# Kernel optimization log

Hardware: AMD Instinct MI355X
Metric: run time of the kernel (lower is better)

Reference implementation:

```python
import jax, jax.numpy as jnp
import numpy as np

B, M, D = 8, 1024, 1024
H = 16
HD = D // H  # 64
F = 4096

def layer_norm(x, gamma, beta, eps=1e-5):
    mu = jnp.mean(x, axis=-1, keepdims=True)
    var = jnp.var(x, axis=-1, keepdims=True)
    return (x - mu) * jax.lax.rsqrt(var + eps) * gamma + beta

def setup_inputs() -> dict:
    key = jax.random.key(0)
    ks = jax.random.split(key, 16)
    s = 0.02
    return {
        "h": jax.random.normal(ks[0], (B, M, D), jnp.float32),
        "h_all": jax.random.normal(ks[1], (B, M, D), jnp.float32),
        "Wq": jax.random.normal(ks[2], (D, D), jnp.float32) * s,
        "Wk": jax.random.normal(ks[3], (D, D), jnp.float32) * s,
        "Wv": jax.random.normal(ks[4], (D, D), jnp.float32) * s,
        "Wo": jax.random.normal(ks[5], (D, D), jnp.float32) * s,
        "W1": jax.random.normal(ks[6], (D, F), jnp.float32) * s,
        "b1": jnp.zeros((F,), jnp.float32),
        "W2": jax.random.normal(ks[7], (F, D), jnp.float32) * s,
        "b2": jnp.zeros((D,), jnp.float32),
        "g1": jnp.ones((D,), jnp.float32),
        "be1": jnp.zeros((D,), jnp.float32),
        "g2": jnp.ones((D,), jnp.float32),
        "be2": jnp.zeros((D,), jnp.float32),
    }

def reference(h, h_all, Wq, Wk, Wv, Wo, W1, b1, W2, b2, g1, be1, g2, be2):
    Bx, Mx, Dx = h.shape
    # projections (no bias, per nn.Linear(bias=False))
    q = (h @ Wq).reshape(Bx, Mx, H, HD)        # [B,M,H,hd]
    k = (h_all @ Wk).reshape(Bx, -1, H, HD)    # [B,N,H,hd]
    v = (h_all @ Wv).reshape(Bx, -1, H, HD)
    # attention: scale by sqrt(head_dim) as in SeqAttention(hidden_size=head_dim)
    scores = jnp.einsum('bqhd,bkhd->bhqk', q, k) / jnp.sqrt(jnp.float32(HD))
    attn = jax.nn.softmax(scores, axis=-1)
    ctx = jnp.einsum('bhqk,bkhd->bqhd', attn, v).reshape(Bx, Mx, Dx)
    attn_out = ctx @ Wo
    # post-norm residual 1
    h1 = layer_norm(h + attn_out, g1, be1)
    # FFN
    ff = jax.nn.relu(h1 @ W1 + b1) @ W2 + b2
    # post-norm residual 2
    out = layer_norm(h1 + ff, g2, be2)
    return out
```

## Files before the change

### kernel.cpp

```cpp
#include <hip/hip_runtime.h>
#include <hip/hip_bf16.h>

#define ROWS 8192
#define DD   1024
#define HH   16
#define HD   64
#define FF   4096

typedef __attribute__((ext_vector_type(4))) float f32x4;
typedef __attribute__((ext_vector_type(8))) __bf16 bf16x8;

static __device__ __forceinline__ unsigned short f2bf(float f) {
  unsigned u = __float_as_uint(f);
  u += 0x7fffu + ((u >> 16) & 1u);
  return (unsigned short)(u >> 16);
}

static __device__ __forceinline__ float bf2f(unsigned short u) {
  return __uint_as_float(((unsigned)u) << 16);
}

static __device__ __forceinline__ unsigned cvtpk_bf16(float lo, float hi) {
  unsigned r;
  asm("v_cvt_pk_bf16_f32 %0, %1, %2" : "=v"(r) : "v"(lo), "v"(hi));
  return r;
}

static __device__ __forceinline__ f32x4 mfma16(bf16x8 a, bf16x8 b, f32x4 c) {
  return __builtin_amdgcn_mfma_f32_16x16x32_bf16(a, b, c, 0, 0, 0);
}

#define GLOAD16(gp, lp) __builtin_amdgcn_global_load_lds( \
    (__attribute__((address_space(1))) void*)(gp), \
    (__attribute__((address_space(3))) void*)(lp), 16, 0, 0)

__global__ __launch_bounds__(256) void prep_k(
    const float* __restrict__ h, const float* __restrict__ hall,
    const float* __restrict__ Wq, const float* __restrict__ Wk,
    const float* __restrict__ Wv, const float* __restrict__ Wo,
    const float* __restrict__ W1, const float* __restrict__ W2,
    unsigned short* __restrict__ hb, unsigned short* __restrict__ hab,
    unsigned short* __restrict__ wqt, unsigned short* __restrict__ wkvt,
    unsigned short* __restrict__ wot, unsigned short* __restrict__ w1t,
    unsigned short* __restrict__ w2t) {
  __shared__ float tile[32][33];
  const int bid = blockIdx.x;
  const int tid = threadIdx.x;

  if (bid < 16384) {
    const float* src = (bid < 8192) ? h : hall;
    unsigned short* dst = (bid < 8192) ? hb : hab;
    int i = (bid & 8191) * 256 + tid;
    float4 v = ((const float4*)src)[i];
    ushort4 o;
    o.x = f2bf(v.x); o.y = f2bf(v.y); o.z = f2bf(v.z); o.w = f2bf(v.w);
    ((ushort4*)dst)[i] = o;
    return;
  }

  int r = bid - 16384;
  const float* src; unsigned short* dst; int R, C, bx, by;
  if (r < 4096) {
    int which = r >> 10, idx = r & 1023;
    R = C = 1024; bx = idx & 31; by = idx >> 5;
    if (which == 0) { src = Wq; dst = wqt; }
    else if (which == 1) { src = Wk; dst = wkvt; }
    else if (which == 2) { src = Wv; dst = wkvt + (size_t)DD * DD; }
    else { src = Wo; dst = wot; }
  } else if (r < 8192) {
    int idx = r - 4096;
    R = 1024; C = 4096; bx = idx & 127; by = idx >> 7;
    src = W1; dst = w1t;
  } else {
    int idx = r - 8192;
    R = 4096; C = 1024; bx = idx & 31; by = idx >> 5;
    src = W2; dst = w2t;
  }
  const int tx = tid & 31, ty = tid >> 5;
  #pragma unroll
  for (int i = 0; i < 32; i += 8)
    tile[ty + i][tx] = src[(size_t)(by * 32 + ty + i) * C + bx * 32 + tx];
  __syncthreads();
  #pragma unroll
  for (int i = 0; i < 32; i += 8)
    dst[(size_t)(bx * 32 + ty + i) * R + by * 32 + tx] = f2bf(tile[tx][ty + i]);
}

template <int BM, int MODE, int KS = 1>
__global__ __launch_bounds__(512, 2) void gemm256(
    const unsigned short* __restrict__ A, const unsigned short* __restrict__ BT,
    const float* __restrict__ bias, void* __restrict__ Cout, void* __restrict__ Cout2,
    int Ni, int Ki, int nbx) {
  constexpr int MR = BM / 32;

  const int tid  = threadIdx.x;
  const int lane = tid & 63;
  const int wid  = tid >> 6;
  const int wm   = wid >> 2;
  const int wn   = wid & 3;
  const int lr   = lane & 15;
  const int kq   = lane >> 4;

  const int nwg = gridDim.x;
  const int cpx = nwg >> 3;
  const int wg  = (int)blockIdx.x;
  const int swz = (wg & 7) * cpx + (wg >> 3);
  const int perk = nwg / KS;
  const int kh   = swz / perk;
  const int swzr = swz % perk;
  const int bx = swzr % nbx, by = swzr / nbx;
  const int brow = by * BM, bcol = bx * 256;
  const int Kc   = Ki / KS;
  const int kbase = kh * Kc;

  f32x4 acc[MR][4] = {};
  const int NT = Kc >> 6;

  if constexpr (BM == 256) {
    __shared__ unsigned short As[2 * 2 * 256 * 32];
    __shared__ unsigned short Bs[2 * 2 * 256 * 32];

    const int srow0 = tid >> 2;
    const int csw   = ((tid & 3) ^ ((tid >> 3) & 3)) * 8;
    const size_t sA0 = (size_t)(brow + srow0) * Ki + kbase + csw;
    const size_t sB0 = (size_t)(bcol + srow0) * Ki + kbase + csw;
    const int coff = ((kq ^ ((lr >> 1) & 3)) << 4);

    auto stageu = [&](int srcT, int db, int ks) {
      const size_t so = (size_t)srcT * 64 + ks * 32;
      char* la = (char*)As + (db * 2 + ks) * 16384 + wid * 1024;
      char* lb = (char*)Bs + (db * 2 + ks) * 16384 + wid * 1024;
      GLOAD16(A + sA0 + so, la);
      GLOAD16(A + sA0 + so + (size_t)128 * Ki, la + 8192);
      GLOAD16(BT + sB0 + so, lb);
      GLOAD16(BT + sB0 + so + (size_t)128 * Ki, lb + 8192);
    };

    stageu(0, 0, 0);
    stageu(0, 0, 1);
    stageu(1, 1, 0);

    #pragma unroll 1
    for (int t = 0; t < NT; ++t) {
      const int d = t & 1;
      #pragma unroll
      for (int p = 0; p < 2; ++p) {
        asm volatile("s_waitcnt vmcnt(8)" ::: "memory");
        __builtin_amdgcn_s_barrier();
        __builtin_amdgcn_sched_barrier(0);
        const char* ab = (const char*)As + (d * 2 + p) * 16384;
        const char* bb = (const char*)Bs + (d * 2 + p) * 16384;
        bf16x8 af[8], bfv[4];
        #pragma unroll
        for (int m = 0; m < 8; ++m)
          af[m] = *(const bf16x8*)(ab + (wm * 128 + m * 16 + lr) * 64 + coff);
        #pragma unroll
        for (int n = 0; n < 4; ++n)
          bfv[n] = *(const bf16x8*)(bb + (wn * 64 + n * 16 + lr) * 64 + coff);
        if (p == 0) {
          const int ts = (t + 1 < NT) ? t + 1 : NT - 1;
          stageu(ts, (t + 1) & 1, 1);
        } else {
          const int ts = (t + 2 < NT) ? t + 2 : NT - 1;
          stageu(ts, d, 0);
        }
        __builtin_amdgcn_s_setprio(1);
        #pragma unroll
        for (int m = 0; m < 8; ++m)
          #pragma unroll
          for (int n = 0; n < 4; ++n)
            acc[m][n] = mfma16(af[m], bfv[n], acc[m][n]);
        __builtin_amdgcn_s_setprio(0);
      }
    }
    asm volatile("s_waitcnt vmcnt(0)" ::: "memory");
  } else {
    __shared__ unsigned short As[2][BM * 64];
    __shared__ unsigned short Bs[2][256 * 64];
    const int axor = (lr & 7) << 4;
    const int srow = wid * 8 + (lane >> 3);
    const int scol = ((lane & 7) * 8) ^ ((srow & 7) << 3);
    size_t offA[BM / 64], offB[4];
    #pragma unroll
    for (int L = 0; L < BM / 64; ++L)
      offA[L] = (size_t)(brow + L * 64 + srow) * Ki + kbase + scol;
    #pragma unroll
    for (int L = 0; L < 4; ++L)
      offB[L] = (size_t)(bcol + L * 64 + srow) * Ki + kbase + scol;

    auto stage = [&](int t, int d) {
      #pragma unroll
      for (int L = 0; L < BM / 64; ++L)
        GLOAD16(A + offA[L] + t * 64, (char*)As[d] + L * 8192 + wid * 1024);
      #pragma unroll
      for (int L = 0; L < 4; ++L)
        GLOAD16(BT + offB[L] + t * 64, (char*)Bs[d] + L * 8192 + wid * 1024);
    };

    stage(0, 0);
    stage(1, 1);

    #pragma unroll 1
    for (int t = 0; t < NT; ++t) {
      const int d = t & 1;
      asm volatile("s_waitcnt vmcnt(6)" ::: "memory");
      __builtin_amdgcn_s_barrier();
      __builtin_amdgcn_sched_barrier(0);

      const unsigned short* as = As[d];
      const unsigned short* bs = Bs[d];
      #pragma unroll
      for (int kk = 0; kk < 2; ++kk) {
        bf16x8 af[MR], bfv[4];
        #pragma unroll
        for (int m = 0; m < MR; ++m)
          af[m] = *(const bf16x8*)((const char*)as +
              (wm * (BM / 2) + m * 16 + lr) * 128 + ((kk * 64 + kq * 16) ^ axor));
        #pragma unroll
        for (int n = 0; n < 4; ++n)
          bfv[n] = *(const bf16x8*)((const char*)bs +
              (wn * 64 + n * 16 + lr) * 128 + ((kk * 64 + kq * 16) ^ axor));
        #pragma unroll
        for (int m = 0; m < MR; ++m)
          #pragma unroll
          for (int n = 0; n < 4; ++n)
            acc[m][n] = mfma16(af[m], bfv[n], acc[m][n]);
      }

      asm volatile("s_waitcnt lgkmcnt(0)" ::: "memory");
      __builtin_amdgcn_s_barrier();
      __builtin_amdgcn_sched_barrier(0);
      const int ts = (t + 2 < NT) ? t + 2 : NT - 1;
      stage(ts, d);
    }
  }

  #pragma unroll
  for (int m = 0; m < MR; ++m) {
    #pragma unroll
    for (int n = 0; n < 4; ++n) {
      const int r0 = brow + wm * (BM / 2) + m * 16 + kq * 4;
      const int c  = bcol + wn * 64 + n * 16 + lr;
      if constexpr (MODE == 4) {
        if (c < 1024) {
          #pragma unroll
          for (int e = 0; e < 4; ++e)
            ((unsigned short*)Cout)[(size_t)(r0 + e) * 1024 + c] = f2bf(acc[m][n][e]);
        } else {
          const int cc = c - 1024;
          const int bq = r0 >> 10;
          const int tok = r0 & 1023;
          ushort4 pk;
          pk.x = f2bf(acc[m][n][0]); pk.y = f2bf(acc[m][n][1]);
          pk.z = f2bf(acc[m][n][2]); pk.w = f2bf(acc[m][n][3]);
          *(ushort4*)((unsigned short*)Cout2 + ((size_t)bq * 1024 + cc) * 1024 + tok) = pk;
        }
      } else if constexpr (MODE == 5) {
        if (kh == 0) {
          const float bv = bias[c];
          #pragma unroll
          for (int e = 0; e < 4; ++e)
            ((float*)Cout)[(size_t)(r0 + e) * Ni + c] = acc[m][n][e] + bv;
        } else {
          #pragma unroll
          for (int e = 0; e < 4; ++e)
            ((unsigned short*)Cout2)[(size_t)(r0 + e) * Ni + c] = f2bf(acc[m][n][e]);
        }
      } else {
        const float bv = (MODE == 2 || MODE == 3) ? bias[c] : 0.0f;
        #pragma unroll
        for (int e = 0; e < 4; ++e) {
          float v = acc[m][n][e] + bv;
          if (MODE == 2) v = fmaxf(v, 0.0f);
          if (MODE == 0 || MODE == 2)
            ((unsigned short*)Cout)[(size_t)(r0 + e) * Ni + c] = f2bf(v);
          else
            ((float*)Cout)[(size_t)(r0 + e) * Ni + c] = v;
        }
      }
    }
  }
}

__global__ __launch_bounds__(512, 6) void attn_k(
    const unsigned short* __restrict__ q, const unsigned short* __restrict__ k,
    const unsigned short* __restrict__ vT, unsigned short* __restrict__ ctx) {
  __shared__ unsigned short Ks[2][64 * 64];
  __shared__ unsigned short Vt[2][64 * 64];
  __shared__ unsigned short Ps[8][16 * 64];
  const int tid = threadIdx.x;
  const int lane = tid & 63;
  const int wid = tid >> 6;
  const int bh = blockIdx.x;
  const int b = bh >> 4, h = bh & 15;
  const int qrow0 = blockIdx.y * 128 + wid * 16;
  const size_t tokbase = (size_t)b * 1024;
  const int lr = lane & 15, kq = lane >> 4;

  const int srow = tid >> 3;
  const int scol = ((tid & 7) * 8) ^ ((srow & 7) << 3);
  const unsigned short* kg = k + (tokbase + srow) * 1024 + h * 64 + scol;
  const unsigned short* vg = vT + ((size_t)(b * 16 + h) * 64 + srow) * 1024 + scol;
  const int ldst = tid * 16;

  auto stage = [&](int kt, int d) {
    GLOAD16(kg + (size_t)kt * 64 * 1024, (char*)Ks[d] + ldst);
    GLOAD16(vg + kt * 64, (char*)Vt[d] + ldst);
  };

  bf16x8 aq[2];
  {
    const unsigned short* qp = q + (tokbase + qrow0 + lr) * DD + h * 64 + kq * 8;
    aq[0] = *(const bf16x8*)qp;
    aq[1] = *(const bf16x8*)(qp + 32);
  }

  float l_acc = 0.f;
  f32x4 acc[4] = {};
  const float C = 0.125f * 1.4426950408889634f;
  const unsigned swp = (unsigned)((lr & 7) << 4);
  const unsigned pbase = (unsigned)(lr * 128);

  stage(0, 0);
  stage(1, 1);

  #pragma unroll 2
  for (int kt = 0; kt < 16; ++kt) {
    const int d = kt & 1;
    asm volatile("s_waitcnt vmcnt(2)" ::: "memory");
    __builtin_amdgcn_s_barrier();
    __builtin_amdgcn_sched_barrier(0);

    f32x4 sv[4] = {};
    #pragma unroll
    for (int jb = 0; jb < 4; ++jb)
      #pragma unroll
      for (int ks = 0; ks < 2; ++ks) {
        int row = jb * 16 + lr;
        bf16x8 ak = *(const bf16x8*)((const char*)Ks[d] +
            row * 128 + ((ks * 64 + kq * 16) ^ ((row & 7) << 4)));
        sv[jb] = mfma16(ak, aq[ks], sv[jb]);
      }

    #pragma unroll
    for (int jb = 0; jb < 4; ++jb) {
      float p0 = exp2f(sv[jb][0] * C);
      float p1 = exp2f(sv[jb][1] * C);
      float p2 = exp2f(sv[jb][2] * C);
      float p3 = exp2f(sv[jb][3] * C);
      l_acc += (p0 + p1) + (p2 + p3);
      uint2 w;
      w.x = cvtpk_bf16(p0, p1);
      w.y = cvtpk_bf16(p2, p3);
      unsigned off = pbase + (((unsigned)(jb * 32 + kq * 8)) ^ swp);
      *(uint2*)((char*)Ps[wid] + off) = w;
    }

    #pragma unroll
    for (int ks = 0; ks < 2; ++ks) {
      bf16x8 ap = *(const bf16x8*)((const char*)Ps[wid] +
          lr * 128 + ((ks * 64 + kq * 16) ^ ((lr & 7) << 4)));
      #pragma unroll
      for (int db = 0; db < 4; ++db) {
        int dd = db * 16 + lr;
        bf16x8 bv = *(const bf16x8*)((const char*)Vt[d] +
            dd * 128 + ((ks * 64 + kq * 16) ^ ((dd & 7) << 4)));
        acc[db] = mfma16(bv, ap, acc[db]);
      }
    }

    asm volatile("s_waitcnt lgkmcnt(0)" ::: "memory");
    __builtin_amdgcn_s_barrier();
    __builtin_amdgcn_sched_barrier(0);
    const int ts = (kt + 2 < 16) ? kt + 2 : 15;
    stage(ts, d);
  }

  float l = l_acc + __shfl_xor(l_acc, 16);
  l += __shfl_xor(l, 32);
  const float inv = 1.0f / l;
  unsigned short* cp = ctx + (tokbase + qrow0 + lr) * DD + h * 64 + kq * 4;
  #pragma unroll
  for (int db = 0; db < 4; ++db) {
    ushort4 o;
    o.x = f2bf(acc[db][0] * inv);
    o.y = f2bf(acc[db][1] * inv);
    o.z = f2bf(acc[db][2] * inv);
    o.w = f2bf(acc[db][3] * inv);
    *(ushort4*)(cp + db * 16) = o;
  }
}

__global__ __launch_bounds__(256) void ln_add_bb_k(
    const unsigned short* __restrict__ a, const unsigned short* __restrict__ b,
    const float* __restrict__ gamma, const float* __restrict__ beta,
    unsigned short* __restrict__ outb) {
  int row = blockIdx.x;
  int tid = threadIdx.x;
  size_t base = (size_t)row * 1024 + tid * 4;
  ushort4 va = *(const ushort4*)(a + base);
  ushort4 vb = *(const ushort4*)(b + base);
  float x[4] = {bf2f(va.x) + bf2f(vb.x), bf2f(va.y) + bf2f(vb.y),
                bf2f(va.z) + bf2f(vb.z), bf2f(va.w) + bf2f(vb.w)};
  float s = x[0] + x[1] + x[2] + x[3];
  float sq = x[0] * x[0] + x[1] * x[1] + x[2] * x[2] + x[3] * x[3];
  #pragma unroll
  for (int mk = 1; mk < 64; mk <<= 1) {
    s += __shfl_xor(s, mk);
    sq += __shfl_xor(sq, mk);
  }
  __shared__ float red[8];
  int wid = tid >> 6, lane = tid & 63;
  if (lane == 0) { red[wid] = s; red[4 + wid] = sq; }
  __syncthreads();
  s = red[0] + red[1] + red[2] + red[3];
  sq = red[4] + red[5] + red[6] + red[7];
  float mu = s * (1.0f / 1024.0f);
  float var = sq * (1.0f / 1024.0f) - mu * mu;
  float rs = rsqrtf(var + 1e-5f);
  float4 g = *(const float4*)(gamma + tid * 4);
  float4 be = *(const float4*)(beta + tid * 4);
  ushort4 ob;
  ob.x = f2bf((x[0] - mu) * rs * g.x + be.x);
  ob.y = f2bf((x[1] - mu) * rs * g.y + be.y);
  ob.z = f2bf((x[2] - mu) * rs * g.z + be.z);
  ob.w = f2bf((x[3] - mu) * rs * g.w + be.w);
  *(ushort4*)(outb + base) = ob;
}

__global__ __launch_bounds__(256) void ln3_k(
    const unsigned short* __restrict__ a, const float* __restrict__ b,
    const unsigned short* __restrict__ c,
    const float* __restrict__ gamma, const float* __restrict__ beta,
    float* __restrict__ outf) {
  int row = blockIdx.x;
  int tid = threadIdx.x;
  size_t base = (size_t)row * 1024 + tid * 4;
  ushort4 va = *(const ushort4*)(a + base);
  float4 vb = *(const float4*)(b + base);
  ushort4 vc = *(const ushort4*)(c + base);
  float x[4] = {bf2f(va.x) + vb.x + bf2f(vc.x), bf2f(va.y) + vb.y + bf2f(vc.y),
                bf2f(va.z) + vb.z + bf2f(vc.z), bf2f(va.w) + vb.w + bf2f(vc.w)};
  float s = x[0] + x[1] + x[2] + x[3];
  float sq = x[0] * x[0] + x[1] * x[1] + x[2] * x[2] + x[3] * x[3];
  #pragma unroll
  for (int mk = 1; mk < 64; mk <<= 1) {
    s += __shfl_xor(s, mk);
    sq += __shfl_xor(sq, mk);
  }
  __shared__ float red[8];
  int wid = tid >> 6, lane = tid & 63;
  if (lane == 0) { red[wid] = s; red[4 + wid] = sq; }
  __syncthreads();
  s = red[0] + red[1] + red[2] + red[3];
  sq = red[4] + red[5] + red[6] + red[7];
  float mu = s * (1.0f / 1024.0f);
  float var = sq * (1.0f / 1024.0f) - mu * mu;
  float rs = rsqrtf(var + 1e-5f);
  float4 g = *(const float4*)(gamma + tid * 4);
  float4 be = *(const float4*)(beta + tid * 4);
  float4 o;
  o.x = (x[0] - mu) * rs * g.x + be.x;
  o.y = (x[1] - mu) * rs * g.y + be.y;
  o.z = (x[2] - mu) * rs * g.z + be.z;
  o.w = (x[3] - mu) * rs * g.w + be.w;
  *(float4*)(outf + base) = o;
}

extern "C" void kernel_launch(void* const* d_in, const int* in_sizes, int n_in,
                              void* d_out, int out_size, void* d_ws, size_t ws_size,
                              hipStream_t stream) {
  const float* h    = (const float*)d_in[0];
  const float* hall = (const float*)d_in[1];
  const float* Wq   = (const float*)d_in[2];
  const float* Wk   = (const float*)d_in[3];
  const float* Wv   = (const float*)d_in[4];
  const float* Wo   = (const float*)d_in[5];
  const float* W1   = (const float*)d_in[6];
  const float* b1   = (const float*)d_in[7];
  const float* W2   = (const float*)d_in[8];
  const float* b2   = (const float*)d_in[9];
  const float* g1   = (const float*)d_in[10];
  const float* be1  = (const float*)d_in[11];
  const float* g2   = (const float*)d_in[12];
  const float* be2  = (const float*)d_in[13];

  char* ws = (char*)d_ws;
  size_t off = 0;
  auto alloc = [&](size_t n) { size_t o = off; off += (n + 255) & ~(size_t)255; return o; };
  const size_t hb_o   = alloc((size_t)ROWS * DD * 2);
  const size_t hab_o  = alloc((size_t)ROWS * DD * 2);
  const size_t wqt_o  = alloc((size_t)DD * DD * 2);
  const size_t wkvt_o = alloc((size_t)DD * DD * 4);
  const size_t wot_o  = alloc((size_t)DD * DD * 2);
  const size_t w1t_o  = alloc((size_t)DD * FF * 2);
  const size_t w2t_o  = alloc((size_t)FF * DD * 2);
  const size_t qb_o   = alloc((size_t)ROWS * DD * 2);
  const size_t kb_o   = alloc((size_t)ROWS * DD * 2);
  const size_t vt_o   = alloc((size_t)ROWS * DD * 2);
  const size_t cx_o   = alloc((size_t)ROWS * DD * 2);
  const size_t h1b_o  = alloc((size_t)ROWS * DD * 2);
  const size_t fp1_o  = alloc((size_t)ROWS * DD * 2);

  unsigned short* hb   = (unsigned short*)(ws + hb_o);
  unsigned short* hab  = (unsigned short*)(ws + hab_o);
  unsigned short* wqt  = (unsigned short*)(ws + wqt_o);
  unsigned short* wkvt = (unsigned short*)(ws + wkvt_o);
  unsigned short* wot  = (unsigned short*)(ws + wot_o);
  unsigned short* w1t  = (unsigned short*)(ws + w1t_o);
  unsigned short* w2t  = (unsigned short*)(ws + w2t_o);
  unsigned short* qb   = (unsigned short*)(ws + qb_o);
  unsigned short* kb   = (unsigned short*)(ws + kb_o);
  unsigned short* vTb  = (unsigned short*)(ws + vt_o);
  unsigned short* cxb  = (unsigned short*)(ws + cx_o);
  unsigned short* h1b  = (unsigned short*)(ws + h1b_o);
  unsigned short* fp1b = (unsigned short*)(ws + fp1_o);
  unsigned short* attn_ob = (unsigned short*)(ws + hab_o);
  unsigned short* ff1     = (unsigned short*)(ws + qb_o);
  float*          outf    = (float*)d_out;

  prep_k<<<dim3(16384 + 4096 + 4096 + 4096), 256, 0, stream>>>(
      h, hall, Wq, Wk, Wv, Wo, W1, W2, hb, hab, wqt, wkvt, wot, w1t, w2t);

  gemm256<128, 0><<<dim3(256), 512, 0, stream>>>(hb,  wqt,  nullptr, qb, nullptr, DD,   DD, 4);
  gemm256<256, 4><<<dim3(256), 512, 0, stream>>>(hab, wkvt, nullptr, kb, vTb,    2048, DD, 8);

  attn_k<<<dim3(128, 8), 512, 0, stream>>>(qb, kb, vTb, cxb);

  gemm256<128, 0><<<dim3(256), 512, 0, stream>>>(cxb, wot, nullptr, attn_ob, nullptr, DD, DD, 4);
  ln_add_bb_k<<<ROWS, 256, 0, stream>>>(hb, attn_ob, g1, be1, h1b);

  gemm256<256, 2>   <<<dim3(512), 512, 0, stream>>>(h1b, w1t, b1, ff1, nullptr, FF, DD, 16);
  gemm256<256, 5, 2><<<dim3(256), 512, 0, stream>>>(ff1, w2t, b2, outf, fp1b, DD, FF, 4);

  ln3_k<<<ROWS, 256, 0, stream>>>(h1b, outf, fp1b, g2, be2, outf);
}
```

Before: 360.0 us.

## Restructure 256-row GEMM main loop into four-phase staged pipeline with full-K LDS rows

Changes the BM=256 GEMM path from two 32-wide K halves per stage to a single 64-wide K tile with 128-byte LDS rows and XOR swizzle. The loop is split into four quarter phases, each loading a slice of A fragments and issuing one chunk of global-to-LDS prefetch. B fragments are loaded once per tile, and barriers plus lgkmcnt waits are interleaved with the MFMAs. The goal is finer-grained overlap of loads with MFMA and less register pressure from fragments, at the cost of more barriers per K tile.

```diff
diff --git a/kernel.cpp b/kernel.cpp
--- a/kernel.cpp
+++ b/kernel.cpp
@@ -100,6 +100,7 @@
   const int wn   = wid & 3;
   const int lr   = lane & 15;
   const int kq   = lane >> 4;
+  const int axor = (lr & 7) << 4;
 
   const int nwg = gridDim.x;
   const int cpx = nwg >> 3;
@@ -117,67 +118,84 @@
   const int NT = Kc >> 6;
 
   if constexpr (BM == 256) {
-    __shared__ unsigned short As[2 * 2 * 256 * 32];
-    __shared__ unsigned short Bs[2 * 2 * 256 * 32];
-
-    const int srow0 = tid >> 2;
-    const int csw   = ((tid & 3) ^ ((tid >> 3) & 3)) * 8;
-    const size_t sA0 = (size_t)(brow + srow0) * Ki + kbase + csw;
-    const size_t sB0 = (size_t)(bcol + srow0) * Ki + kbase + csw;
-    const int coff = ((kq ^ ((lr >> 1) & 3)) << 4);
-
-    auto stageu = [&](int srcT, int db, int ks) {
-      const size_t so = (size_t)srcT * 64 + ks * 32;
-      char* la = (char*)As + (db * 2 + ks) * 16384 + wid * 1024;
-      char* lb = (char*)Bs + (db * 2 + ks) * 16384 + wid * 1024;
-      GLOAD16(A + sA0 + so, la);
-      GLOAD16(A + sA0 + so + (size_t)128 * Ki, la + 8192);
-      GLOAD16(BT + sB0 + so, lb);
-      GLOAD16(BT + sB0 + so + (size_t)128 * Ki, lb + 8192);
+    __shared__ unsigned short As[2 * 256 * 64];
+    __shared__ unsigned short Bs[2 * 256 * 64];
+
+    const size_t loff = (size_t)(lane >> 3) * Ki + ((lane & 7) ^ (lane >> 3)) * 8;
+    const unsigned short* Ab = A + (size_t)brow * Ki + kbase;
+    const unsigned short* Bb = BT + (size_t)bcol * Ki + kbase;
+
+    auto stage2 = [&](int qc, int u, int db) {
+      const int ra = ((wid & 4) << 5) + qc * 32 + (wid & 3) * 8;
+      GLOAD16(Ab + (size_t)ra * Ki + u * 64 + loff,
+              (char*)As + db * 32768 + ra * 128);
+      const int rb = qc * 64 + wid * 8;
+      GLOAD16(Bb + (size_t)rb * Ki + u * 64 + loff,
+              (char*)Bs + db * 32768 + rb * 128);
     };
 
-    stageu(0, 0, 0);
-    stageu(0, 0, 1);
-    stageu(1, 1, 0);
+    #pragma unroll
+    for (int qc = 0; qc < 4; ++qc) stage2(qc, 0, 0);
+    {
+      const int u1 = (1 < NT) ? 1 : NT - 1;
+      stage2(0, u1, 1); stage2(1, u1, 1); stage2(2, u1, 1);
+    }
+    asm volatile("s_waitcnt vmcnt(6)" ::: "memory");
+    __builtin_amdgcn_s_barrier();
+    __builtin_amdgcn_sched_barrier(0);
 
     #pragma unroll 1
     for (int t = 0; t < NT; ++t) {
       const int d = t & 1;
+      const char* ab = (const char*)As + d * 32768;
+      const char* bb = (const char*)Bs + d * 32768;
+      bf16x8 bfv[4][2];
       #pragma unroll
-      for (int p = 0; p < 2; ++p) {
-        asm volatile("s_waitcnt vmcnt(8)" ::: "memory");
+      for (int q = 0; q < 4; ++q) {
+        bf16x8 af[2][2];
+        #pragma unroll
+        for (int mm = 0; mm < 2; ++mm)
+          #pragma unroll
+          for (int ks = 0; ks < 2; ++ks)
+            af[mm][ks] = *(const bf16x8*)(ab +
+                (wm * 128 + (q * 2 + mm) * 16 + lr) * 128 +
+                ((ks * 64 + kq * 16) ^ axor));
+        if (q == 0) {
+          #pragma unroll
+          for (int n = 0; n < 4; ++n)
+            #pragma unroll
+            for (int ks = 0; ks < 2; ++ks)
+              bfv[n][ks] = *(const bf16x8*)(bb +
+                  (wn * 64 + n * 16 + lr) * 128 +
+                  ((ks * 64 + kq * 16) ^ axor));
+        }
+        if (q == 0) {
+          stage2(3, (t + 1 < NT) ? t + 1 : NT - 1, (t + 1) & 1);
+        } else {
+          stage2(q - 1, (t + 2 < NT) ? t + 2 : NT - 1, d);
+        }
+        __builtin_amdgcn_sched_barrier(0);
+        __builtin_amdgcn_s_barrier();
+        asm volatile("s_waitcnt lgkmcnt(0)" ::: "memory");
+        __builtin_amdgcn_sched_barrier(0);
+        __builtin_amdgcn_s_setprio(1);
+        #pragma unroll
+        for (int mm = 0; mm < 2; ++mm)
+          #pragma unroll
+          for (int n = 0; n < 4; ++n) {
+            acc[q * 2 + mm][n] = mfma16(af[mm][0], bfv[n][0], acc[q * 2 + mm][n]);
+            acc[q * 2 + mm][n] = mfma16(af[mm][1], bfv[n][1], acc[q * 2 + mm][n]);
+          }
+        __builtin_amdgcn_s_setprio(0);
+        if (q == 3) asm volatile("s_waitcnt vmcnt(6)" ::: "memory");
         __builtin_amdgcn_s_barrier();
         __builtin_amdgcn_sched_barrier(0);
-        const char* ab = (const char*)As + (d * 2 + p) * 16384;
-        const char* bb = (const char*)Bs + (d * 2 + p) * 16384;
-        bf16x8 af[8], bfv[4];
-        #pragma unroll
-        for (int m = 0; m < 8; ++m)
-          af[m] = *(const bf16x8*)(ab + (wm * 128 + m * 16 + lr) * 64 + coff);
-        #pragma unroll
-        for (int n = 0; n < 4; ++n)
-          bfv[n] = *(const bf16x8*)(bb + (wn * 64 + n * 16 + lr) * 64 + coff);
-        if (p == 0) {
-          const int ts = (t + 1 < NT) ? t + 1 : NT - 1;
-          stageu(ts, (t + 1) & 1, 1);
-        } else {
-          const int ts = (t + 2 < NT) ? t + 2 : NT - 1;
-          stageu(ts, d, 0);
-        }
-        __builtin_amdgcn_s_setprio(1);
-        #pragma unroll
-        for (int m = 0; m < 8; ++m)
-          #pragma unroll
-          for (int n = 0; n < 4; ++n)
-            acc[m][n] = mfma16(af[m], bfv[n], acc[m][n]);
-        __builtin_amdgcn_s_setprio(0);
       }
     }
     asm volatile("s_waitcnt vmcnt(0)" ::: "memory");
   } else {
     __shared__ unsigned short As[2][BM * 64];
     __shared__ unsigned short Bs[2][256 * 64];
-    const int axor = (lr & 7) << 4;
     const int srow = wid * 8 + (lane >> 3);
     const int scol = ((lane & 7) * 8) ^ ((srow & 7) << 3);
     size_t offA[BM / 64], offB[4];
```

Measured after the change: 352.7 us. 2.0% less time.
